# Optimization experiments

Hardware: AMD Instinct MI355X
Metric: run time of the kernel (lower is better)

## Reference

```python
import jax, jax.numpy as jnp
import numpy as np

RADIUS = 1.0
NSAMPLE = 8
GROUPS = 8
EPS = 1e-5


def setup_inputs() -> dict:
    key = jax.random.key(0)
    ks = jax.random.split(key, 8)
    b, n_p, dim, C = 4, 4096, 128, 64
    coords = jax.random.normal(ks[0], (b, n_p, 3), jnp.float32)
    xyz2 = jax.random.normal(ks[1], (b, n_p, 3), jnp.float32)
    fmap1 = jax.random.normal(ks[2], (b, dim, n_p), jnp.float32)
    fmap2 = jax.random.normal(ks[3], (b, dim, n_p), jnp.float32)
    conv_w = jax.random.normal(ks[4], (C, 4), jnp.float32) * 0.1
    conv_b = jnp.zeros((C,), jnp.float32)
    gn_gamma = jnp.ones((C,), jnp.float32)
    gn_beta = jnp.zeros((C,), jnp.float32)
    prelu_a = jnp.full((1,), 0.25, jnp.float32)
    out_w = jax.random.normal(ks[5], (C, C), jnp.float32) * 0.1
    out_b = jnp.zeros((C,), jnp.float32)
    return {"coords": coords, "xyz2": xyz2, "fmap1": fmap1, "fmap2": fmap2,
            "conv_w": conv_w, "conv_b": conv_b, "gn_gamma": gn_gamma,
            "gn_beta": gn_beta, "prelu_a": prelu_a, "out_w": out_w, "out_b": out_b}


def ball_query(xyz2, coords, radius, nsample):
    # first-nsample points of xyz2 within `radius` of each query in coords,
    # padded with the first valid index (0 if none) -- matches PointNet++ ball query.
    n = xyz2.shape[1]
    d2 = jnp.sum((coords[:, :, None, :] - xyz2[:, None, :, :]) ** 2, axis=-1)  # [b,m,n]
    j = jnp.arange(n, dtype=jnp.float32)
    score = jnp.where(d2 < radius * radius, -j, -float(n))  # larger score = earlier valid idx
    vals, _ = jax.lax.top_k(score, nsample)  # [b,m,nsample]
    valid = vals > -float(n)
    idx = (-vals).astype(jnp.int32)
    first = jnp.where(valid[..., :1], idx[..., :1], 0)
    return jnp.where(valid, idx, first)  # [b,m,nsample]


def reference(coords, xyz2, fmap1, fmap2, conv_w, conv_b, gn_gamma, gn_beta, prelu_a, out_w, out_b):
    b, n_p, _ = coords.shape
    dim = fmap1.shape[1]
    # corr = fmap1^T fmap2 / sqrt(dim): [b, n_p, n_p]
    corr = jnp.einsum('bdn,bdm->bnm', fmap1, fmap2) / jnp.sqrt(jnp.float32(dim))
    idx = ball_query(xyz2, coords, RADIUS, NSAMPLE)  # [b,n_p,nsample]
    # grouped_xyz: xyz2[idx] - coords -> [b, 3, n_p, nsample]
    gathered = jax.vmap(lambda pts, ind: pts[ind])(xyz2, idx)  # [b,n_p,ns,3]
    grouped_xyz = jnp.transpose(gathered - coords[:, :, None, :], (0, 3, 1, 2))
    # corr gather along source dim
    cur_corr = jnp.take_along_axis(corr, idx, axis=2)[:, None]  # [b,1,n_p,ns]
    feat = jnp.concatenate([cur_corr, grouped_xyz], axis=1)  # [b,4,n_p,ns]
    # 1x1 Conv2d
    x = jnp.einsum('oc,bcns->bons', conv_w, feat) + conv_b[None, :, None, None]
    # GroupNorm(8, 64)
    C = x.shape[1]
    xg = x.reshape(b, GROUPS, C // GROUPS, n_p, NSAMPLE)
    mu = jnp.mean(xg, axis=(2, 3, 4), keepdims=True)
    var = jnp.var(xg, axis=(2, 3, 4), keepdims=True)
    xg = (xg - mu) * jax.lax.rsqrt(var + EPS)
    x = xg.reshape(b, C, n_p, NSAMPLE) * gn_gamma[None, :, None, None] + gn_beta[None, :, None, None]
    # PReLU (single shared slope)
    x = jnp.where(x >= 0, x, prelu_a[0] * x)
    # max over neighbors
    x = jnp.max(x, axis=3)  # [b,64,n_p]
    # 1x1 Conv1d out
    return jnp.einsum('oc,bcn->bon', out_w, x) + out_b[None, :, None]
```

## Files before the change

kernel.cpp:

```cpp
#include <hip/hip_runtime.h>
#include <hip/hip_cooperative_groups.h>
#include <math.h>

namespace cg = cooperative_groups;

#define B 4
#define NP 4096
#define DIM 128
#define CCH 64
#define NS 8

struct TrS { float tile[128][17]; };
struct K2S { float As[16 * 132]; float red[4][14]; };
struct KbS {
  float4 fs4[128]; float4 vs4[256]; float4 ow4[1024];
  float cw[256], cb[64], Av[64], Bv[64], ob[64];
  float red2[8][14], Sm[14], SxA[64], SxxA[64];
};
static_assert(sizeof(KbS) >= sizeof(TrS) && sizeof(KbS) >= sizeof(K2S), "union size");

__global__ __launch_bounds__(256, 4) void fused_all(
    const float* __restrict__ coords, const float* __restrict__ xyz2,
    const float* __restrict__ f1, const float* __restrict__ f2,
    const float* __restrict__ conv_w, const float* __restrict__ conv_b,
    const float* __restrict__ gamma, const float* __restrict__ beta,
    const float* __restrict__ prelu, const float* __restrict__ out_w,
    const float* __restrict__ out_b, float* __restrict__ out,
    float* __restrict__ f2T, float* __restrict__ feat,
    float* __restrict__ parts, int* __restrict__ idxb, int useT) {
  cg::grid_group grid = cg::this_grid();
  __shared__ __align__(16) unsigned char smraw[sizeof(KbS)];
  int blk = blockIdx.x;
  int t = threadIdx.x;

  if (useT) {
    TrS& tr = *reinterpret_cast<TrS*>(smraw);
    int b = blk >> 8;
    int n0 = (blk & 255) * 16;
    const float* s = f2 + (size_t)b * DIM * NP;
    float* dd = f2T + (size_t)b * NP * DIM;
#pragma unroll
    for (int it = 0; it < 2; ++it) {
      int f = t + it * 256;
      int d = f >> 2, ng = f & 3;
      float4 v = *(const float4*)&s[(size_t)d * NP + n0 + ng * 4];
      tr.tile[d][ng * 4 + 0] = v.x;
      tr.tile[d][ng * 4 + 1] = v.y;
      tr.tile[d][ng * 4 + 2] = v.z;
      tr.tile[d][ng * 4 + 3] = v.w;
    }
    __syncthreads();
#pragma unroll
    for (int it = 0; it < 2; ++it) {
      int f = t + it * 256;
      int n = f >> 5, dg = f & 31;
      float4 w;
      w.x = tr.tile[dg * 4 + 0][n];
      w.y = tr.tile[dg * 4 + 1][n];
      w.z = tr.tile[dg * 4 + 2][n];
      w.w = tr.tile[dg * 4 + 3][n];
      *(float4*)&dd[(size_t)(n0 + n) * DIM + dg * 4] = w;
    }
  }

  {
    int wv = t >> 6, lane = t & 63;
#pragma unroll 1
    for (int qi = 0; qi < 4; ++qi) {
      int q = blk * 16 + wv * 4 + qi;
      int b = q >> 12, m = q & (NP - 1);
      const float* cp = coords + ((size_t)b * NP + m) * 3;
      float cx = cp[0], cy = cp[1], cz = cp[2];
      const float* xz = xyz2 + (size_t)b * NP * 3;
      int j0 = lane * 3;
      float px = xz[j0], py = xz[j0 + 1], pz = xz[j0 + 2];
      int cnt = 0, myidx = 0, first = 0;
      for (int c = 0; c < 64 && cnt < NS; ++c) {
        int cn = (c < 63) ? c + 1 : 63;
        int jn = (cn * 64 + lane) * 3;
        float nx = xz[jn], ny = xz[jn + 1], nz = xz[jn + 2];
        float dx = __fsub_rn(cx, px);
        float dy = __fsub_rn(cy, py);
        float dz = __fsub_rn(cz, pz);
        float d2 = __fadd_rn(__fadd_rn(__fmul_rn(dx, dx), __fmul_rn(dy, dy)),
                             __fmul_rn(dz, dz));
        unsigned long long mk = __ballot(d2 < 1.0f);
        while (mk && cnt < NS) {
          int bpos = __ffsll(mk) - 1;
          int jf = c * 64 + bpos;
          if (lane == cnt) myidx = jf;
          if (cnt == 0) first = jf;
          ++cnt;
          mk &= mk - 1;
        }
        px = nx; py = ny; pz = nz;
      }
      if (lane < NS) {
        int v = (lane < cnt) ? myidx : ((cnt > 0) ? first : 0);
        idxb[((size_t)b * NP + m) * NS + lane] = v;
      }
    }
  }

  grid.sync();

  {
    K2S& k2 = *reinterpret_cast<K2S*>(smraw);
    int i = blk;
    int b = (i & 7) >> 1;
    int chunk = ((i >> 3) << 1) | (i & 1);
    int m0 = chunk * 16;
    if (useT) {
#pragma unroll
      for (int pass = 0; pass < 2; ++pass) {
        int d = pass * 64 + (t >> 2);
        int j4 = t & 3;
        float4 v = *(const float4*)&f1[(size_t)(b * DIM + d) * NP + m0 + j4 * 4];
        k2.As[(j4 * 4 + 0) * 132 + d] = v.x;
        k2.As[(j4 * 4 + 1) * 132 + d] = v.y;
        k2.As[(j4 * 4 + 2) * 132 + d] = v.z;
        k2.As[(j4 * 4 + 3) * 132 + d] = v.w;
      }
    }
    __syncthreads();

    int g = t >> 3;
    int l = t & 7;
    size_t ibase = ((size_t)b * NP + m0) * NS;
    int idv[4];
#pragma unroll
    for (int r = 0; r < 4; ++r) idv[r] = idxb[ibase + r * 32 + g];

    float pm[14];
#pragma unroll
    for (int k = 0; k < 14; ++k) pm[k] = 0.f;

#pragma unroll
    for (int r = 0; r < 4; ++r) {
      int pi = r * 32 + g;
      int m = pi >> 3, s = pi & 7;
      int id = idv[r];
      float acc = 0.f;
      if (useT) {
        const float4* brow = (const float4*)(f2T + ((size_t)b * NP + id) * DIM);
        const float4* arow = (const float4*)&k2.As[m * 132];
#pragma unroll
        for (int k = 0; k < 4; ++k) {
          float4 y = brow[l + 8 * k];
          float4 x = arow[l + 8 * k];
          acc += x.x * y.x + x.y * y.y + x.z * y.z + x.w * y.w;
        }
      } else {
#pragma unroll
        for (int k = 0; k < 4; ++k) {
#pragma unroll
          for (int c = 0; c < 4; ++c) {
            int d = (l + 8 * k) * 4 + c;
            acc += f1[(size_t)(b * DIM + d) * NP + m0 + m] *
                   f2[(size_t)(b * DIM + d) * NP + id];
          }
        }
      }
      acc += __shfl_xor(acc, 1);
      acc += __shfl_xor(acc, 2);
      acc += __shfl_xor(acc, 4);
      float corr = acc * 0.08838834764831843f;
      const float* cp = coords + ((size_t)b * NP + m0 + m) * 3;
      const float* xp = xyz2 + ((size_t)b * NP + id) * 3;
      float dx = xp[0] - cp[0], dy = xp[1] - cp[1], dz = xp[2] - cp[2];
      if (l == 0) {
        float4 fv;
        fv.x = corr; fv.y = dx; fv.z = dy; fv.w = dz;
        ((float4*)feat)[((size_t)b * NP + m0 + m) * NS + s] = fv;
      }
      pm[0] += corr; pm[1] += dx; pm[2] += dy; pm[3] += dz;
      pm[4] += corr * corr; pm[5] += corr * dx; pm[6] += corr * dy;
      pm[7] += corr * dz; pm[8] += dx * dx; pm[9] += dx * dy;
      pm[10] += dx * dz; pm[11] += dy * dy; pm[12] += dy * dz; pm[13] += dz * dz;
    }
#pragma unroll
    for (int k = 0; k < 14; ++k) {
      float v = pm[k];
#pragma unroll
      for (int off = 32; off; off >>= 1) v += __shfl_xor(v, off);
      pm[k] = v;
    }
    int lane = t & 63, wvv = t >> 6;
    if (lane == 0) {
#pragma unroll
      for (int k = 0; k < 14; ++k) k2.red[wvv][k] = pm[k];
    }
    __syncthreads();
    if (t < 14) {
      float ssum = (k2.red[0][t] + k2.red[1][t] + k2.red[2][t] + k2.red[3][t]) * 0.125f;
      parts[((size_t)b * 256 + chunk) * 14 + t] = ssum;
    }
  }

  grid.sync();

  {
    KbS& kb = *reinterpret_cast<KbS*>(smraw);
    int b = blk >> 8;
    int n0 = (blk & 255) * 16;
    if (t < 128) kb.fs4[t] = ((const float4*)(feat + ((size_t)b * NP + n0) * 32))[t];
    {
      const float4* src = (const float4*)out_w;
#pragma unroll
      for (int k = 0; k < 4; ++k) {
        int i4 = t + k * 256;
        int oo = i4 >> 4, gg = i4 & 15;
        kb.ow4[oo * 16 + (gg ^ ((oo >> 2) & 7))] = src[i4];
      }
    }
    kb.cw[t] = conv_w[t];
    if (t < 64) {
      kb.cb[t] = conv_b[t];
      kb.ob[t] = out_b[t];
    }
    if (t < 112) {
      int k = t % 14, jg = t / 14;
      float s = 0.f;
      const float* pp = parts + ((size_t)b * 256 + jg * 32) * 14 + k;
      for (int j = 0; j < 32; ++j) s += pp[j * 14];
      kb.red2[jg][k] = s;
    }
    float alpha = prelu[0];
    __syncthreads();
    if (t < 14) {
      float s = 0.f;
#pragma unroll
      for (int jg = 0; jg < 8; ++jg) s += kb.red2[jg][t];
      kb.Sm[t] = s;
    }
    __syncthreads();
    if (t < 64) {
      int o = t;
      float w0 = kb.cw[o * 4 + 0], w1 = kb.cw[o * 4 + 1];
      float w2 = kb.cw[o * 4 + 2], w3 = kb.cw[o * 4 + 3];
      float bo = kb.cb[o];
      const float cnt = (float)(NP * NS);
      float wS1 = w0 * kb.Sm[0] + w1 * kb.Sm[1] + w2 * kb.Sm[2] + w3 * kb.Sm[3];
      float q = w0 * w0 * kb.Sm[4] + w1 * w1 * kb.Sm[8] + w2 * w2 * kb.Sm[11] +
                w3 * w3 * kb.Sm[13] +
                2.f * (w0 * w1 * kb.Sm[5] + w0 * w2 * kb.Sm[6] + w0 * w3 * kb.Sm[7] +
                       w1 * w2 * kb.Sm[9] + w1 * w3 * kb.Sm[10] + w2 * w3 * kb.Sm[12]);
      kb.SxA[o] = wS1 + bo * cnt;
      kb.SxxA[o] = q + 2.f * bo * wS1 + bo * bo * cnt;
    }
    __syncthreads();
    if (t < 64) {
      int o = t, g = o >> 3;
      const float cnt = (float)(NP * NS);
      float sm = 0.f, s2 = 0.f;
#pragma unroll
      for (int k = 0; k < 8; ++k) {
        sm += kb.SxA[g * 8 + k];
        s2 += kb.SxxA[g * 8 + k];
      }
      float mean = sm / (cnt * 8.f);
      float e2 = s2 / (cnt * 8.f);
      float var = e2 - mean * mean;
      float inv = rsqrtf(var + 1e-5f);
      float A = gamma[o] * inv;
      kb.Av[o] = A;
      kb.Bv[o] = beta[o] - mean * A;
    }
    __syncthreads();

    {
      int o = t & 63;
      int pw = t >> 6;
      float w0 = kb.cw[o * 4 + 0], w1 = kb.cw[o * 4 + 1];
      float w2 = kb.cw[o * 4 + 2], w3 = kb.cw[o * 4 + 3];
      float A = kb.Av[o], Bc = kb.Bv[o], bb = kb.cb[o];
      float* vsf = (float*)kb.vs4;
#pragma unroll
      for (int i = 0; i < 4; ++i) {
        int p = pw * 4 + i;
        float mx = -INFINITY;
#pragma unroll
        for (int s = 0; s < NS; ++s) {
          float4 f = kb.fs4[p * 8 + s];
          float x = fmaf(w0, f.x, fmaf(w1, f.y, fmaf(w2, f.z, fmaf(w3, f.w, bb))));
          float y = fmaf(A, x, Bc);
          y = (y >= 0.f) ? y : alpha * y;
          mx = fmaxf(mx, y);
        }
        vsf[(p * 16 + ((o >> 2) ^ ((p >> 2) & 7))) * 4 + (o & 3)] = mx;
      }
    }
    __syncthreads();

    {
      int ti = t >> 3;
      int tj = t & 7;
      float acc[2][2];
#pragma unroll
      for (int oi = 0; oi < 2; ++oi)
#pragma unroll
        for (int pj = 0; pj < 2; ++pj) acc[oi][pj] = 0.f;
#pragma unroll
      for (int g = 0; g < 16; ++g) {
        float4 vv[2], ww[2];
#pragma unroll
        for (int pj = 0; pj < 2; ++pj) {
          int p = tj * 2 + pj;
          vv[pj] = kb.vs4[p * 16 + (g ^ ((p >> 2) & 7))];
        }
#pragma unroll
        for (int oi = 0; oi < 2; ++oi) {
          int oo = ti * 2 + oi;
          ww[oi] = kb.ow4[oo * 16 + (g ^ ((oo >> 2) & 7))];
        }
#pragma unroll
        for (int oi = 0; oi < 2; ++oi)
#pragma unroll
          for (int pj = 0; pj < 2; ++pj) {
            acc[oi][pj] = fmaf(ww[oi].x, vv[pj].x, acc[oi][pj]);
            acc[oi][pj] = fmaf(ww[oi].y, vv[pj].y, acc[oi][pj]);
            acc[oi][pj] = fmaf(ww[oi].z, vv[pj].z, acc[oi][pj]);
            acc[oi][pj] = fmaf(ww[oi].w, vv[pj].w, acc[oi][pj]);
          }
      }
#pragma unroll
      for (int oi = 0; oi < 2; ++oi) {
        int oo = ti * 2 + oi;
        float bb = kb.ob[oo];
        float2 r;
        r.x = acc[oi][0] + bb;
        r.y = acc[oi][1] + bb;
        *(float2*)&out[((size_t)b * CCH + oo) * NP + n0 + tj * 2] = r;
      }
    }
  }
}

__global__ __launch_bounds__(256) void kA_bq_transpose(
    const float* __restrict__ coords, const float* __restrict__ xyz2,
    int* __restrict__ idxb, const float* __restrict__ f2,
    float* __restrict__ o2) {
  int blk = blockIdx.x;
  int t = threadIdx.x;
  __shared__ float tile[128][33];
  if (blk < B * NP) {
    int b = blk >> 12, m = blk & (NP - 1);
    int wv = t >> 6, lane = t & 63;
    const float* cp = coords + ((size_t)b * NP + m) * 3;
    float cx = cp[0], cy = cp[1], cz = cp[2];
    const float* xz = xyz2 + (size_t)b * NP * 3;
    int base = wv * 1024;
    int j0 = (base + lane) * 3;
    float px = xz[j0], py = xz[j0 + 1], pz = xz[j0 + 2];
    int cnt = 0, myidx = 0;
    for (int c = 0; c < 16 && cnt < NS; ++c) {
      int cn = (c < 15) ? c + 1 : 15;
      int jn = (base + cn * 64 + lane) * 3;
      float nx = xz[jn], ny = xz[jn + 1], nz = xz[jn + 2];
      float dx = __fsub_rn(cx, px);
      float dy = __fsub_rn(cy, py);
      float dz = __fsub_rn(cz, pz);
      float d2 = __fadd_rn(__fadd_rn(__fmul_rn(dx, dx), __fmul_rn(dy, dy)),
                           __fmul_rn(dz, dz));
      unsigned long long mk = __ballot(d2 < 1.0f);
      while (mk && cnt < NS) {
        int bpos = __ffsll(mk) - 1;
        int jf = base + c * 64 + bpos;
        if (lane == cnt) myidx = jf;
        ++cnt;
        mk &= mk - 1;
      }
      px = nx; py = ny; pz = nz;
    }
    __shared__ int sidx[4][NS];
    __shared__ int scnt[4];
    if (lane < NS) sidx[wv][lane] = myidx;
    if (lane == 0) scnt[wv] = cnt;
    __syncthreads();
    if (t < NS) {
      int c0 = scnt[0], c1 = scnt[1], c2 = scnt[2], c3 = scnt[3];
      int total = c0 + c1 + c2 + c3;
      int v;
      if (t < c0) v = sidx[0][t];
      else if (t < c0 + c1) v = sidx[1][t - c0];
      else if (t < c0 + c1 + c2) v = sidx[2][t - c0 - c1];
      else if (t < total) v = sidx[3][t - c0 - c1 - c2];
      else v = (c0 > 0) ? sidx[0][0]
             : (c1 > 0) ? sidx[1][0]
             : (c2 > 0) ? sidx[2][0]
             : (c3 > 0) ? sidx[3][0] : 0;
      idxb[((size_t)b * NP + m) * NS + t] = v;
    }
  } else {
    int tb = blk - B * NP;
    int b = tb >> 7;
    int n0 = (tb & 127) * 32;
    const float* s = f2 + (size_t)b * DIM * NP;
    float* d = o2 + (size_t)b * NP * DIM;
    int dr = t >> 3;
    int ng = t & 7;
#pragma unroll
    for (int k = 0; k < 4; ++k) {
      int dd = dr + 32 * k;
      float4 v = *(const float4*)&s[(size_t)dd * NP + n0 + ng * 4];
      tile[dd][ng * 4 + 0] = v.x;
      tile[dd][ng * 4 + 1] = v.y;
      tile[dd][ng * 4 + 2] = v.z;
      tile[dd][ng * 4 + 3] = v.w;
    }
    __syncthreads();
    int n = t >> 3;
#pragma unroll
    for (int k = 0; k < 4; ++k) {
      int d0 = (t & 7) * 4 + 32 * k;
      float4 w;
      w.x = tile[d0 + 0][n];
      w.y = tile[d0 + 1][n];
      w.z = tile[d0 + 2][n];
      w.w = tile[d0 + 3][n];
      *(float4*)&d[(size_t)(n0 + n) * DIM + d0] = w;
    }
  }
}

__global__ __launch_bounds__(256) void k2_corrfeat(
    const float* __restrict__ f1, const float* __restrict__ f2T,
    const float* __restrict__ coords, const float* __restrict__ xyz2,
    const int* __restrict__ idxb, float* __restrict__ feat,
    float* __restrict__ parts, int trans) {
  int i = blockIdx.x;
  int b = (i & 7) >> 1;
  int chunk = ((i >> 3) << 1) | (i & 1);
  int m0 = chunk * 16;
  int t = threadIdx.x;
  __shared__ float As[16 * 132];
  __shared__ float red[4][14];
  if (trans) {
#pragma unroll
    for (int pass = 0; pass < 2; ++pass) {
      int d = pass * 64 + (t >> 2);
      int j4 = t & 3;
      float4 v = *(const float4*)&f1[(size_t)(b * DIM + d) * NP + m0 + j4 * 4];
      As[(j4 * 4 + 0) * 132 + d] = v.x;
      As[(j4 * 4 + 1) * 132 + d] = v.y;
      As[(j4 * 4 + 2) * 132 + d] = v.z;
      As[(j4 * 4 + 3) * 132 + d] = v.w;
    }
  }
  __syncthreads();
  int g = t >> 3;
  int l = t & 7;
  size_t ibase = ((size_t)b * NP + m0) * NS;
  int idv[4];
#pragma unroll
  for (int r = 0; r < 4; ++r) idv[r] = idxb[ibase + r * 32 + g];
  float pm[14];
#pragma unroll
  for (int k = 0; k < 14; ++k) pm[k] = 0.f;
#pragma unroll
  for (int r = 0; r < 4; ++r) {
    int pi = r * 32 + g;
    int m = pi >> 3, s = pi & 7;
    int id = idv[r];
    float acc = 0.f;
    if (trans) {
      const float4* brow = (const float4*)(f2T + ((size_t)b * NP + id) * DIM);
      const float4* arow = (const float4*)&As[m * 132];
#pragma unroll
      for (int k = 0; k < 4; ++k) {
        float4 y = brow[l + 8 * k];
        float4 x = arow[l + 8 * k];
        acc += x.x * y.x + x.y * y.y + x.z * y.z + x.w * y.w;
      }
    } else {
#pragma unroll
      for (int k = 0; k < 4; ++k) {
#pragma unroll
        for (int c = 0; c < 4; ++c) {
          int d = (l + 8 * k) * 4 + c;
          acc += f1[(size_t)(b * DIM + d) * NP + m0 + m] *
                 f2T[(size_t)(b * DIM + d) * NP + id];
        }
      }
    }
    acc += __shfl_xor(acc, 1);
    acc += __shfl_xor(acc, 2);
    acc += __shfl_xor(acc, 4);
    float corr = acc * 0.08838834764831843f;
    const float* cp = coords + ((size_t)b * NP + m0 + m) * 3;
    const float* xp = xyz2 + ((size_t)b * NP + id) * 3;
    float dx = xp[0] - cp[0], dy = xp[1] - cp[1], dz = xp[2] - cp[2];
    if (l == 0) {
      float4 fv;
      fv.x = corr; fv.y = dx; fv.z = dy; fv.w = dz;
      ((float4*)feat)[((size_t)b * NP + m0 + m) * NS + s] = fv;
    }
    pm[0] += corr; pm[1] += dx; pm[2] += dy; pm[3] += dz;
    pm[4] += corr * corr; pm[5] += corr * dx; pm[6] += corr * dy;
    pm[7] += corr * dz; pm[8] += dx * dx; pm[9] += dx * dy;
    pm[10] += dx * dz; pm[11] += dy * dy; pm[12] += dy * dz; pm[13] += dz * dz;
  }
#pragma unroll
  for (int k = 0; k < 14; ++k) {
    float v = pm[k];
#pragma unroll
    for (int off = 32; off; off >>= 1) v += __shfl_xor(v, off);
    pm[k] = v;
  }
  int lane = t & 63, wvv = t >> 6;
  if (lane == 0) {
#pragma unroll
    for (int k = 0; k < 14; ++k) red[wvv][k] = pm[k];
  }
  __syncthreads();
  if (t < 14) {
    float ssum = (red[0][t] + red[1][t] + red[2][t] + red[3][t]) * 0.125f;
    parts[((size_t)b * 256 + chunk) * 14 + t] = ssum;
  }
}

__global__ __launch_bounds__(256) void kB_out(
    const float* __restrict__ feat, const float* __restrict__ parts,
    const float* __restrict__ conv_w, const float* __restrict__ conv_b,
    const float* __restrict__ gamma, const float* __restrict__ beta,
    const float* __restrict__ prelu, const float* __restrict__ out_w,
    const float* __restrict__ out_b, float* __restrict__ out) {
  int b = blockIdx.x >> 8;
  int n0 = (blockIdx.x & 255) * 16;
  __shared__ float4 fs4[16 * 8];
  __shared__ float4 vs4[16 * 16];
  __shared__ float4 ow4[64 * 16];
  __shared__ float cw[256], cb_[64], Av[64], Bv[64], ob_[64];
  __shared__ float red2[8][14];
  __shared__ float Sm[14];
  __shared__ float SxA[64], SxxA[64];
  int t = threadIdx.x;
  if (t < 128) fs4[t] = ((const float4*)(feat + ((size_t)b * NP + n0) * 32))[t];
  {
    const float4* src = (const float4*)out_w;
#pragma unroll
    for (int k = 0; k < 4; ++k) {
      int i4 = t + k * 256;
      int oo = i4 >> 4, gg = i4 & 15;
      ow4[oo * 16 + (gg ^ ((oo >> 2) & 7))] = src[i4];
    }
  }
  cw[t] = conv_w[t];
  if (t < 64) {
    cb_[t] = conv_b[t];
    ob_[t] = out_b[t];
  }
  if (t < 112) {
    int k = t % 14, jg = t / 14;
    float s = 0.f;
    const float* pp = parts + ((size_t)b * 256 + jg * 32) * 14 + k;
    for (int j = 0; j < 32; ++j) s += pp[j * 14];
    red2[jg][k] = s;
  }
  float alpha = prelu[0];
  __syncthreads();
  if (t < 14) {
    float s = 0.f;
#pragma unroll
    for (int jg = 0; jg < 8; ++jg) s += red2[jg][t];
    Sm[t] = s;
  }
  __syncthreads();
  if (t < 64) {
    int o = t;
    float w0 = cw[o * 4 + 0], w1 = cw[o * 4 + 1];
    float w2 = cw[o * 4 + 2], w3 = cw[o * 4 + 3];
    float bo = cb_[o];
    const float cnt = (float)(NP * NS);
    float wS1 = w0 * Sm[0] + w1 * Sm[1] + w2 * Sm[2] + w3 * Sm[3];
    float q = w0 * w0 * Sm[4] + w1 * w1 * Sm[8] + w2 * w2 * Sm[11] +
              w3 * w3 * Sm[13] +
              2.f * (w0 * w1 * Sm[5] + w0 * w2 * Sm[6] + w0 * w3 * Sm[7] +
                     w1 * w2 * Sm[9] + w1 * w3 * Sm[10] + w2 * w3 * Sm[12]);
    SxA[o] = wS1 + bo * cnt;
    SxxA[o] = q + 2.f * bo * wS1 + bo * bo * cnt;
  }
  __syncthreads();
  if (t < 64) {
    int o = t, g = o >> 3;
    const float cnt = (float)(NP * NS);
    float sm = 0.f, s2 = 0.f;
#pragma unroll
    for (int k = 0; k < 8; ++k) {
      sm += SxA[g * 8 + k];
      s2 += SxxA[g * 8 + k];
    }
    float mean = sm / (cnt * 8.f);
    float e2 = s2 / (cnt * 8.f);
    float var = e2 - mean * mean;
    float inv = rsqrtf(var + 1e-5f);
    float A = gamma[o] * inv;
    Av[o] = A;
    Bv[o] = beta[o] - mean * A;
  }
  __syncthreads();
  {
    int o = t & 63;
    int pw = t >> 6;
    float w0 = cw[o * 4 + 0], w1 = cw[o * 4 + 1];
    float w2 = cw[o * 4 + 2], w3 = cw[o * 4 + 3];
    float A = Av[o], Bc = Bv[o], bb = cb_[o];
    float* vsf = (float*)vs4;
#pragma unroll
    for (int i = 0; i < 4; ++i) {
      int p = pw * 4 + i;
      float mx = -INFINITY;
#pragma unroll
      for (int s = 0; s < NS; ++s) {
        float4 f = fs4[p * 8 + s];
        float x = fmaf(w0, f.x, fmaf(w1, f.y, fmaf(w2, f.z, fmaf(w3, f.w, bb))));
        float y = fmaf(A, x, Bc);
        y = (y >= 0.f) ? y : alpha * y;
        mx = fmaxf(mx, y);
      }
      vsf[(p * 16 + ((o >> 2) ^ ((p >> 2) & 7))) * 4 + (o & 3)] = mx;
    }
  }
  __syncthreads();
  {
    int ti = t >> 3;
    int tj = t & 7;
    float acc[2][2];
#pragma unroll
    for (int oi = 0; oi < 2; ++oi)
#pragma unroll
      for (int pj = 0; pj < 2; ++pj) acc[oi][pj] = 0.f;
#pragma unroll
    for (int g = 0; g < 16; ++g) {
      float4 vv[2], ww[2];
#pragma unroll
      for (int pj = 0; pj < 2; ++pj) {
        int p = tj * 2 + pj;
        vv[pj] = vs4[p * 16 + (g ^ ((p >> 2) & 7))];
      }
#pragma unroll
      for (int oi = 0; oi < 2; ++oi) {
        int oo = ti * 2 + oi;
        ww[oi] = ow4[oo * 16 + (g ^ ((oo >> 2) & 7))];
      }
#pragma unroll
      for (int oi = 0; oi < 2; ++oi)
#pragma unroll
        for (int pj = 0; pj < 2; ++pj) {
          acc[oi][pj] = fmaf(ww[oi].x, vv[pj].x, acc[oi][pj]);
          acc[oi][pj] = fmaf(ww[oi].y, vv[pj].y, acc[oi][pj]);
          acc[oi][pj] = fmaf(ww[oi].z, vv[pj].z, acc[oi][pj]);
          acc[oi][pj] = fmaf(ww[oi].w, vv[pj].w, acc[oi][pj]);
        }
    }
#pragma unroll
    for (int oi = 0; oi < 2; ++oi) {
      int oo = ti * 2 + oi;
      float bb = ob_[oo];
      float2 r;
      r.x = acc[oi][0] + bb;
      r.y = acc[oi][1] + bb;
      *(float2*)&out[((size_t)b * CCH + oo) * NP + n0 + tj * 2] = r;
    }
  }
}

extern "C" void kernel_launch(void* const* d_in, const int* in_sizes, int n_in,
                              void* d_out, int out_size, void* d_ws, size_t ws_size,
                              hipStream_t stream) {
  const float* coords = (const float*)d_in[0];
  const float* xyz2 = (const float*)d_in[1];
  const float* fmap1 = (const float*)d_in[2];
  const float* fmap2 = (const float*)d_in[3];
  const float* conv_w = (const float*)d_in[4];
  const float* conv_b = (const float*)d_in[5];
  const float* gamma = (const float*)d_in[6];
  const float* beta = (const float*)d_in[7];
  const float* prelu = (const float*)d_in[8];
  const float* out_w = (const float*)d_in[9];
  const float* out_b = (const float*)d_in[10];
  float* out = (float*)d_out;
  float* ws = (float*)d_ws;

  const size_t BND = (size_t)B * NP * DIM;
  const size_t FEAT = (size_t)B * NP * NS * 4;
  const size_t PARTS = (size_t)B * 256 * 14;
  size_t needT = (BND + FEAT + PARTS + 512) * sizeof(float) +
                 (size_t)B * NP * NS * sizeof(int);
  int useT = (ws_size >= needT) ? 1 : 0;

  float* f2T = ws;
  float* featp = useT ? (f2T + BND) : ws;
  float* parts = featp + FEAT;
  int* idxp = (int*)(parts + PARTS + 512);

  int maxBlocks = 0;
  hipError_t oe = hipOccupancyMaxActiveBlocksPerMultiprocessor(
      &maxBlocks, fused_all, 256, 0);
  if (oe == hipSuccess && maxBlocks >= 4) {
    void* args[] = {(void*)&coords, (void*)&xyz2,   (void*)&fmap1,
                    (void*)&fmap2,  (void*)&conv_w, (void*)&conv_b,
                    (void*)&gamma,  (void*)&beta,   (void*)&prelu,
                    (void*)&out_w,  (void*)&out_b,  (void*)&out,
                    (void*)&f2T,    (void*)&featp,  (void*)&parts,
                    (void*)&idxp,   (void*)&useT};
    hipError_t le = hipLaunchCooperativeKernel(
        fused_all, dim3(1024), dim3(256), args, 0, stream);
    if (le == hipSuccess) return;
  }

  int nblk = B * NP + (useT ? (B * (NP / 32)) : 0);
  kA_bq_transpose<<<dim3(nblk), dim3(256), 0, stream>>>(coords, xyz2, idxp,
                                                        fmap2, f2T);
  k2_corrfeat<<<dim3(1024), dim3(256), 0, stream>>>(
      fmap1, useT ? f2T : fmap2, coords, xyz2, idxp, featp, parts, useT);
  kB_out<<<dim3(B * (NP / 16)), dim3(256), 0, stream>>>(
      featp, parts, conv_w, conv_b, gamma, beta, prelu, out_w, out_b, out);
}
```

Before: 50.21 us.

## Keep ball-query indices and features in shared memory across fused phases

Remaps the ball-query and output phases so each block handles the same 16 queries it uses in the correlation phase. Neighbor indices and the per-neighbor feature vectors then stay in LDS instead of being written to and read back from global memory around the grid syncs. The ballot loop now assigns each hit's slot with a popcount prefix instead of a serial per-bit loop, and the transpose tile gets padding with rotating offsets to reduce LDS bank conflicts. LDS use per block grows, since the index and feature arrays sit outside the phase union, which could affect occupancy at 4 blocks per CU.

```diff
diff --git a/kernel.cpp b/kernel.cpp
--- a/kernel.cpp
+++ b/kernel.cpp
@@ -10,14 +10,18 @@
 #define CCH 64
 #define NS 8
 
-struct TrS { float tile[128][17]; };
+struct TrS { float tile[128][31]; };
 struct K2S { float As[16 * 132]; float red[4][14]; };
-struct KbS {
-  float4 fs4[128]; float4 vs4[256]; float4 ow4[1024];
+struct K3S {
+  float4 vs4[256]; float4 ow4[1024];
   float cw[256], cb[64], Av[64], Bv[64], ob[64];
   float red2[8][14], Sm[14], SxA[64], SxxA[64];
 };
-static_assert(sizeof(KbS) >= sizeof(TrS) && sizeof(KbS) >= sizeof(K2S), "union size");
+struct SM {
+  float4 fs4[128];
+  int sidx[128];
+  union { TrS tr; K2S k2; K3S k3; } u;
+};
 
 __global__ __launch_bounds__(256, 4) void fused_all(
     const float* __restrict__ coords, const float* __restrict__ xyz2,
@@ -26,15 +30,16 @@
     const float* __restrict__ gamma, const float* __restrict__ beta,
     const float* __restrict__ prelu, const float* __restrict__ out_w,
     const float* __restrict__ out_b, float* __restrict__ out,
-    float* __restrict__ f2T, float* __restrict__ feat,
-    float* __restrict__ parts, int* __restrict__ idxb, int useT) {
+    float* __restrict__ f2T, float* __restrict__ parts, int useT) {
   cg::grid_group grid = cg::this_grid();
-  __shared__ __align__(16) unsigned char smraw[sizeof(KbS)];
+  __shared__ SM sm;
   int blk = blockIdx.x;
   int t = threadIdx.x;
+  int bq = (blk & 7) >> 1;
+  int chunk = ((blk >> 3) << 1) | (blk & 1);
+  int m0 = chunk * 16;
 
   if (useT) {
-    TrS& tr = *reinterpret_cast<TrS*>(smraw);
     int b = blk >> 8;
     int n0 = (blk & 255) * 16;
     const float* s = f2 + (size_t)b * DIM * NP;
@@ -44,37 +49,39 @@
       int f = t + it * 256;
       int d = f >> 2, ng = f & 3;
       float4 v = *(const float4*)&s[(size_t)d * NP + n0 + ng * 4];
-      tr.tile[d][ng * 4 + 0] = v.x;
-      tr.tile[d][ng * 4 + 1] = v.y;
-      tr.tile[d][ng * 4 + 2] = v.z;
-      tr.tile[d][ng * 4 + 3] = v.w;
+      int aw = 5 * (d >> 5);
+      sm.u.tr.tile[d][ng * 4 + 0 + aw] = v.x;
+      sm.u.tr.tile[d][ng * 4 + 1 + aw] = v.y;
+      sm.u.tr.tile[d][ng * 4 + 2 + aw] = v.z;
+      sm.u.tr.tile[d][ng * 4 + 3 + aw] = v.w;
     }
     __syncthreads();
 #pragma unroll
     for (int it = 0; it < 2; ++it) {
       int f = t + it * 256;
       int n = f >> 5, dg = f & 31;
+      int ar = 5 * (dg >> 3);
       float4 w;
-      w.x = tr.tile[dg * 4 + 0][n];
-      w.y = tr.tile[dg * 4 + 1][n];
-      w.z = tr.tile[dg * 4 + 2][n];
-      w.w = tr.tile[dg * 4 + 3][n];
+      w.x = sm.u.tr.tile[dg * 4 + 0][n + ar];
+      w.y = sm.u.tr.tile[dg * 4 + 1][n + ar];
+      w.z = sm.u.tr.tile[dg * 4 + 2][n + ar];
+      w.w = sm.u.tr.tile[dg * 4 + 3][n + ar];
       *(float4*)&dd[(size_t)(n0 + n) * DIM + dg * 4] = w;
     }
   }
 
   {
     int wv = t >> 6, lane = t & 63;
+    const float* xz = xyz2 + (size_t)bq * NP * 3;
 #pragma unroll 1
     for (int qi = 0; qi < 4; ++qi) {
-      int q = blk * 16 + wv * 4 + qi;
-      int b = q >> 12, m = q & (NP - 1);
-      const float* cp = coords + ((size_t)b * NP + m) * 3;
+      int m = m0 + wv * 4 + qi;
+      const float* cp = coords + ((size_t)bq * NP + m) * 3;
       float cx = cp[0], cy = cp[1], cz = cp[2];
-      const float* xz = xyz2 + (size_t)b * NP * 3;
       int j0 = lane * 3;
       float px = xz[j0], py = xz[j0 + 1], pz = xz[j0 + 2];
-      int cnt = 0, myidx = 0, first = 0;
+      int cnt = 0, first = 0;
+      bool any = false;
       for (int c = 0; c < 64 && cnt < NS; ++c) {
         int cn = (c < 63) ? c + 1 : 63;
         int jn = (cn * 64 + lane) * 3;
@@ -84,32 +91,29 @@
         float dz = __fsub_rn(cz, pz);
         float d2 = __fadd_rn(__fadd_rn(__fmul_rn(dx, dx), __fmul_rn(dy, dy)),
                              __fmul_rn(dz, dz));
-        unsigned long long mk = __ballot(d2 < 1.0f);
-        while (mk && cnt < NS) {
-          int bpos = __ffsll(mk) - 1;
-          int jf = c * 64 + bpos;
-          if (lane == cnt) myidx = jf;
-          if (cnt == 0) first = jf;
-          ++cnt;
-          mk &= mk - 1;
+        bool hit = d2 < 1.0f;
+        unsigned long long mk = __ballot(hit);
+        if (mk) {
+          int rank = cnt + __popcll(mk & ((1ull << lane) - 1ull));
+          if (hit && rank < NS) sm.sidx[(wv * 4 + qi) * NS + rank] = c * 64 + lane;
+          if (!any) {
+            first = c * 64 + (__ffsll((long long)mk) - 1);
+            any = true;
+          }
+          cnt += __popcll(mk);
         }
         px = nx; py = ny; pz = nz;
       }
-      if (lane < NS) {
-        int v = (lane < cnt) ? myidx : ((cnt > 0) ? first : 0);
-        idxb[((size_t)b * NP + m) * NS + lane] = v;
-      }
+      if (lane < NS && lane >= cnt)
+        sm.sidx[(wv * 4 + qi) * NS + lane] = first;
     }
   }
 
   grid.sync();
 
   {
-    K2S& k2 = *reinterpret_cast<K2S*>(smraw);
-    int i = blk;
-    int b = (i & 7) >> 1;
-    int chunk = ((i >> 3) << 1) | (i & 1);
-    int m0 = chunk * 16;
+    K2S& k2 = sm.u.k2;
+    int b = bq;
     if (useT) {
 #pragma unroll
       for (int pass = 0; pass < 2; ++pass) {
@@ -126,10 +130,9 @@
 
     int g = t >> 3;
     int l = t & 7;
-    size_t ibase = ((size_t)b * NP + m0) * NS;
     int idv[4];
 #pragma unroll
-    for (int r = 0; r < 4; ++r) idv[r] = idxb[ibase + r * 32 + g];
+    for (int r = 0; r < 4; ++r) idv[r] = sm.sidx[r * 32 + g];
 
     float pm[14];
 #pragma unroll
@@ -138,7 +141,7 @@
 #pragma unroll
     for (int r = 0; r < 4; ++r) {
       int pi = r * 32 + g;
-      int m = pi >> 3, s = pi & 7;
+      int m = pi >> 3;
       int id = idv[r];
       float acc = 0.f;
       if (useT) {
@@ -171,7 +174,7 @@
       if (l == 0) {
         float4 fv;
         fv.x = corr; fv.y = dx; fv.z = dy; fv.w = dz;
-        ((float4*)feat)[((size_t)b * NP + m0 + m) * NS + s] = fv;
+        sm.fs4[pi] = fv;
       }
       pm[0] += corr; pm[1] += dx; pm[2] += dy; pm[3] += dz;
       pm[4] += corr * corr; pm[5] += corr * dx; pm[6] += corr * dy;
@@ -193,17 +196,16 @@
     __syncthreads();
     if (t < 14) {
       float ssum = (k2.red[0][t] + k2.red[1][t] + k2.red[2][t] + k2.red[3][t]) * 0.125f;
-      parts[((size_t)b * 256 + chunk) * 14 + t] = ssum;
+      parts[((size_t)bq * 256 + chunk) * 14 + t] = ssum;
     }
   }
 
   grid.sync();
 
   {
-    KbS& kb = *reinterpret_cast<KbS*>(smraw);
-    int b = blk >> 8;
-    int n0 = (blk & 255) * 16;
-    if (t < 128) kb.fs4[t] = ((const float4*)(feat + ((size_t)b * NP + n0) * 32))[t];
+    K3S& kb = sm.u.k3;
+    int b = bq;
+    int n0 = m0;
     {
       const float4* src = (const float4*)out_w;
 #pragma unroll
@@ -252,13 +254,13 @@
     if (t < 64) {
       int o = t, g = o >> 3;
       const float cnt = (float)(NP * NS);
-      float sm = 0.f, s2 = 0.f;
+      float sm_ = 0.f, s2 = 0.f;
 #pragma unroll
       for (int k = 0; k < 8; ++k) {
-        sm += kb.SxA[g * 8 + k];
+        sm_ += kb.SxA[g * 8 + k];
         s2 += kb.SxxA[g * 8 + k];
       }
-      float mean = sm / (cnt * 8.f);
+      float mean = sm_ / (cnt * 8.f);
       float e2 = s2 / (cnt * 8.f);
       float var = e2 - mean * mean;
       float inv = rsqrtf(var + 1e-5f);
@@ -281,7 +283,7 @@
         float mx = -INFINITY;
 #pragma unroll
         for (int s = 0; s < NS; ++s) {
-          float4 f = kb.fs4[p * 8 + s];
+          float4 f = sm.fs4[p * 8 + s];
           float x = fmaf(w0, f.x, fmaf(w1, f.y, fmaf(w2, f.z, fmaf(w3, f.w, bb))));
           float y = fmaf(A, x, Bc);
           y = (y >= 0.f) ? y : alpha * y;
@@ -702,8 +704,7 @@
                     (void*)&fmap2,  (void*)&conv_w, (void*)&conv_b,
                     (void*)&gamma,  (void*)&beta,   (void*)&prelu,
                     (void*)&out_w,  (void*)&out_b,  (void*)&out,
-                    (void*)&f2T,    (void*)&featp,  (void*)&parts,
-                    (void*)&idxp,   (void*)&useT};
+                    (void*)&f2T,    (void*)&parts,  (void*)&useT};
     hipError_t le = hipLaunchCooperativeKernel(
         fused_all, dim3(1024), dim3(256), args, 0, stream);
     if (le == hipSuccess) return;
```

After: 50.22 us. Within noise of the previous version (+0.0%).
